# Kernel tuning notes

Hardware: AMD Instinct MI355X
Metric: run time of the kernel (lower is better)

The kernel has to match this reference:

```python
import jax, jax.numpy as jnp
import numpy as np

LOG_EPS = -1000.0
NEG_INF = -1e9  # stand-in for -inf (numerically identical in fp32 LSE, grad-safe)
NOISE_SCALE = 2.0


def setup_inputs() -> dict:
    key = jax.random.key(0)
    ks = jax.random.split(key, 8)
    B, I, J = 2, 64, 512
    Dt, Dm, A = 512, 80, 128
    return {
        "text_embeddings": jax.random.normal(ks[0], (B, I, Dt), jnp.float32),
        "mel_embeddings": jax.random.normal(ks[1], (B, J, Dm), jnp.float32),
        "noise": jax.random.normal(ks[2], (B, I, J), jnp.float32),
        "text_mask": jnp.ones((B, I), dtype=bool),
        "mel_mask": jnp.ones((B, J), dtype=bool),
        "mel_w": jax.random.normal(ks[3], (A, Dm), jnp.float32) * 0.05,
        "mel_b": jax.random.normal(ks[4], (A,), jnp.float32) * 0.05,
        "text_w": jax.random.normal(ks[5], (A, Dt), jnp.float32) * 0.05,
        "v_w": jax.random.normal(ks[6], (A,), jnp.float32) * (1.0 / np.sqrt(A)),
        "v_b": jax.random.normal(ks[7], (1,), jnp.float32) * 0.05,
    }


def _forward(text_embeddings, mel_embeddings, noise, text_mask, mel_mask,
             mel_w, mel_b, text_w, v_w, v_b):
    B, I, _ = text_embeddings.shape
    J = mel_embeddings.shape[1]
    lse = jax.nn.logsumexp

    # --- energy: additive tanh attention + sigmoid(energy + noise) -> (B, I, J)
    pm = mel_embeddings @ mel_w.T + mel_b              # (B, J, A)
    pt = text_embeddings @ text_w.T                    # (B, I, A)
    energy = jnp.tanh(pm[:, None, :, :] + pt[:, :, None, :]) @ v_w + v_b[0]
    energy = jax.nn.sigmoid(energy + noise * NOISE_SCALE)

    # --- log conditional prob P(B_i = j | B_{i-1} = k): (B, I, J, K=J)
    jj = jnp.arange(J)
    tri = jj[:, None] <= jj[None, :]                   # invalid where j <= k (monotone boundaries)
    invalid = (tri[None, None]
               | ~text_mask[:, :, None, None]
               | ~mel_mask[:, None, :, None]
               | ~mel_mask[:, None, None, :])
    e4 = jnp.where(invalid, LOG_EPS, energy[..., None])
    lcp = e4 - lse(e4, axis=2, keepdims=True)          # normalize over j
    # P(B_i >= j | B_{i-1} = k): reversed cumulative logsumexp over j
    geq = jnp.flip(jax.lax.cumlogsumexp(jnp.flip(lcp, 2), axis=2), 2)
    geq = jnp.where(invalid, LOG_EPS, geq)

    # --- forward DP in log domain: B_ij of shape (B, I+1, J+1)
    Jm = (mel_mask.sum(1) - text_mask.sum(1)).max()
    row0 = jnp.full((B, J + 1), NEG_INF).at[:, 0].set(0.0)
    jcol = jnp.arange(J + 1)[None, :]

    def step(prev, xs):
        i, lcp_i = xs                                   # lcp_i: (B, J, K)
        contrib = lse(prev[:, None, :-1] + lcp_i, axis=-1)   # (B, J), fills cols 1..J
        row = jnp.concatenate([jnp.full((B, 1), NEG_INF), contrib], axis=1)
        row = jnp.where((jcol >= i) & (jcol < Jm + i + 2), row, NEG_INF)
        return row, row

    _, rows = jax.lax.scan(step, row0,
                           (jnp.arange(1, I + 1), jnp.swapaxes(lcp, 0, 1)))
    Bij = jnp.concatenate([row0[:, None, :], jnp.swapaxes(rows, 0, 1)], axis=1)

    # --- interval probability P(B_{i-1} < j <= B_i): (B, I, J)
    prob = Bij[:, :-1, :-1]                             # log P(B_{i-1} = k)
    soft = lse(prob[:, :, :, None] + jnp.swapaxes(geq, 2, 3), axis=2)

    # --- expanded text embeddings: (B, J, D_text)
    align_mask = text_mask[:, :, None] & mel_mask[:, None, :]
    expanded = jnp.einsum('bij,bid->bjd', jnp.exp(soft) * align_mask, text_embeddings)
    return soft, expanded


def reference(text_embeddings, mel_embeddings, noise, text_mask, mel_mask,
              mel_w, mel_b, text_w, v_w, v_b):
    return _forward(text_embeddings, mel_embeddings, noise, text_mask, mel_mask,
                    mel_w, mel_b, text_w, v_w, v_b)
```

## Files before the change

kernel.cpp:

```cpp
#include <hip/hip_runtime.h>
#include <math.h>

#define NB 2
#define NI 64
#define NJ 512
#define NDT 512
#define NDM 80
#define NA 128

#define NEG9    (-1000000000.0f)
#define LOGEPS  (-1000.0f)
#define IDENT   (-1.0e30f)
#define LN512   (6.2383246250f)
#define LN2F    (0.69314718056f)
#define INVLN2  (1.44269504089f)
#define LOGEPS2 (-1442.6950409f)

__device__ __forceinline__ float lse2(float a, float b) {
    float m = fmaxf(a, b);
    float d = fabsf(a - b);
    return m + __logf(1.0f + __expf(-d));
}

struct Pair { float m, s; };

__device__ __forceinline__ Pair pcomb(Pair a, Pair b) {
    float mm = fmaxf(a.m, b.m);
    float e  = exp2f(-fabsf(a.m - b.m));
    bool agt = a.m >= b.m;
    float hi = agt ? a.s : b.s;
    float lo = agt ? b.s : a.s;
    return {mm, fmaf(lo, e, hi)};
}

template<int CTRL, int RM>
__device__ __forceinline__ float dpp_lse(float s) {
    int v = __builtin_amdgcn_update_dpp(__float_as_int(IDENT), __float_as_int(s),
                                        CTRL, RM, 0xf, false);
    return lse2(s, __int_as_float(v));
}
template<int CTRL, int RM>
__device__ __forceinline__ Pair dpp_pcomb(Pair x) {
    int bm = __builtin_amdgcn_update_dpp(__float_as_int(IDENT), __float_as_int(x.m),
                                         CTRL, RM, 0xf, false);
    int bs = __builtin_amdgcn_update_dpp(0, __float_as_int(x.s),
                                         CTRL, RM, 0xf, false);
    Pair b{__int_as_float(bm), __int_as_float(bs)};
    return pcomb(x, b);
}

__device__ __forceinline__ float wave_lse_scan(float x) {
    x = dpp_lse<0x111, 0xf>(x);
    x = dpp_lse<0x112, 0xf>(x);
    x = dpp_lse<0x114, 0xf>(x);
    x = dpp_lse<0x118, 0xf>(x);
    x = dpp_lse<0x142, 0xa>(x);
    x = dpp_lse<0x143, 0xc>(x);
    return x;
}
__device__ __forceinline__ Pair wave_pair_scan(Pair x) {
    x = dpp_pcomb<0x111, 0xf>(x);
    x = dpp_pcomb<0x112, 0xf>(x);
    x = dpp_pcomb<0x114, 0xf>(x);
    x = dpp_pcomb<0x118, 0xf>(x);
    x = dpp_pcomb<0x142, 0xa>(x);
    x = dpp_pcomb<0x143, 0xc>(x);
    return x;
}

__device__ __forceinline__ float bcast63(float x) {
    return __int_as_float(__builtin_amdgcn_readlane(__float_as_int(x), 63));
}
__device__ __forceinline__ Pair readp63(Pair x) {
    return { __int_as_float(__builtin_amdgcn_readlane(__float_as_int(x.m), 63)),
             __int_as_float(__builtin_amdgcn_readlane(__float_as_int(x.s), 63)) };
}
__device__ __forceinline__ Pair shflup1(Pair x) {
    return { __shfl_up(x.m, 1, 64), __shfl_up(x.s, 1, 64) };
}

__device__ __forceinline__ void sklansky8(const float* q, float* ls) {
    ls[0]=q[0]; ls[2]=q[2]; ls[4]=q[4]; ls[6]=q[6];
    ls[1]=lse2(q[0],q[1]); ls[3]=lse2(q[2],q[3]);
    ls[5]=lse2(q[4],q[5]); ls[7]=lse2(q[6],q[7]);
    ls[2]=lse2(ls[1],ls[2]); ls[3]=lse2(ls[1],ls[3]);
    ls[6]=lse2(ls[5],ls[6]); ls[7]=lse2(ls[5],ls[7]);
    ls[4]=lse2(ls[3],ls[4]); ls[5]=lse2(ls[3],ls[5]);
    ls[6]=lse2(ls[3],ls[6]); ls[7]=lse2(ls[3],ls[7]);
}
__device__ __forceinline__ void sklansky8p(const Pair* q, Pair* ls) {
    ls[0]=q[0]; ls[2]=q[2]; ls[4]=q[4]; ls[6]=q[6];
    ls[1]=pcomb(q[0],q[1]); ls[3]=pcomb(q[2],q[3]);
    ls[5]=pcomb(q[4],q[5]); ls[7]=pcomb(q[6],q[7]);
    ls[2]=pcomb(ls[1],ls[2]); ls[3]=pcomb(ls[1],ls[3]);
    ls[6]=pcomb(ls[5],ls[6]); ls[7]=pcomb(ls[5],ls[7]);
    ls[4]=pcomb(ls[3],ls[4]); ls[5]=pcomb(ls[3],ls[5]);
    ls[6]=pcomb(ls[3],ls[6]); ls[7]=pcomb(ls[3],ls[7]);
}

__global__ __launch_bounds__(128) void k_proj(const float* __restrict__ text,
                                              const float* __restrict__ mel,
                                              const float* __restrict__ mel_w,
                                              const float* __restrict__ mel_b,
                                              const float* __restrict__ text_w,
                                              float* __restrict__ pmT,
                                              float* __restrict__ pt) {
    __shared__ float row[NDT];
    int blk = blockIdx.x;
    int tid = threadIdx.x;
    if (blk < NB * NJ) {
        int b = blk >> 9, j = blk & (NJ - 1);
        if (tid < NDM) row[tid] = mel[(b * NJ + j) * NDM + tid];
        __syncthreads();
        float acc = mel_b[tid];
        #pragma unroll 8
        for (int k = 0; k < NDM; ++k) acc = fmaf(row[k], mel_w[tid * NDM + k], acc);
        pmT[(b * NA + tid) * NJ + j] = acc;
    } else {
        int blk2 = blk - NB * NJ;
        int b = blk2 >> 6, i = blk2 & (NI - 1);
        for (int k = tid; k < NDT; k += 128) row[k] = text[(b * NI + i) * NDT + k];
        __syncthreads();
        float acc = 0.0f;
        #pragma unroll 8
        for (int k = 0; k < NDT; ++k) acc = fmaf(row[k], text_w[tid * NDT + k], acc);
        pt[(b * NI + i) * NA + tid] = acc;
    }
}

__global__ __launch_bounds__(512) void k_energy(const float* __restrict__ pmT,
                                                const float* __restrict__ pt,
                                                const float* __restrict__ v_w,
                                                const float* __restrict__ v_b,
                                                const float* __restrict__ noise,
                                                float* __restrict__ energy) {
    int bi = blockIdx.x;
    int j = threadIdx.x;
    int b = bi >> 6;
    __shared__ float pts[NA];
    __shared__ float vws[NA];
    if (j < NA) { pts[j] = pt[bi * NA + j]; vws[j] = v_w[j]; }
    __syncthreads();
    float acc = 0.0f;
    const float* pmb = pmT + b * NA * NJ + j;
    #pragma unroll 4
    for (int a = 0; a < NA; ++a) {
        float x = pmb[a * NJ] + pts[a];
        float t = __expf(2.0f * x);
        float th = 1.0f - 2.0f / (t + 1.0f);
        acc = fmaf(th, vws[a], acc);
    }
    float x = acc + v_b[0] + 2.0f * noise[bi * NJ + j];
    energy[bi * NJ + j] = 1.0f / (1.0f + __expf(-x));
}

__global__ __launch_bounds__(64) void k_suffix(const float* __restrict__ energy,
                                               float* __restrict__ T,
                                               float* __restrict__ denom) {
    int bi = blockIdx.x;
    int lane = threadIdx.x;
    const float4* er = (const float4*)(energy + bi * NJ);
    float4 v0 = er[lane * 2], v1 = er[lane * 2 + 1];
    float q[8] = {v0.x, v0.y, v0.z, v0.w, v1.x, v1.y, v1.z, v1.w};
    float ss[8];
    ss[7] = q[7];
    #pragma unroll
    for (int t = 6; t >= 0; --t) ss[t] = lse2(q[t], ss[t + 1]);
    float tot = ss[0];
    #pragma unroll
    for (int off = 1; off < 64; off <<= 1) {
        float o = __shfl_down(tot, off, 64);
        if (lane + off < 64) tot = lse2(tot, o);
    }
    float offS = __shfl_down(tot, 1, 64);
    if (lane == 63) offS = IDENT;
    float Tl[8];
    #pragma unroll
    for (int t = 0; t < 8; ++t) Tl[t] = lse2(ss[t], offS);
    float4* Tr = (float4*)(T + bi * NJ);
    Tr[lane * 2]     = make_float4(Tl[0], Tl[1], Tl[2], Tl[3]);
    Tr[lane * 2 + 1] = make_float4(Tl[4], Tl[5], Tl[6], Tl[7]);
    float nextT0 = __shfl_down(Tl[0], 1, 64);
    float dn[8];
    #pragma unroll
    for (int t = 0; t < 7; ++t) dn[t] = Tl[t + 1];
    dn[7] = (lane == 63) ? (LOGEPS + LN512) : nextT0;
    float4* dr = (float4*)(denom + bi * NJ);
    dr[lane * 2]     = make_float4(dn[0], dn[1], dn[2], dn[3]);
    dr[lane * 2 + 1] = make_float4(dn[4], dn[5], dn[6], dn[7]);
}

__global__ __launch_bounds__(64) void k_scan(const float* __restrict__ denom,
                                             const float* __restrict__ energy,
                                             float* __restrict__ prob) {
    int b = blockIdx.x;
    int lane = threadIdx.x;
    int f = lane * 8;
    Pair prev[8];
    #pragma unroll
    for (int t = 0; t < 8; ++t) prev[t] = {NEG9, 1.0f};
    if (lane == 0) prev[0] = {0.0f, 1.0f};
    float* prow = prob + b * NI * NJ;
    {
        float4* pr = (float4*)prow;
        pr[lane * 2]     = make_float4(prev[0].m, prev[1].m, prev[2].m, prev[3].m);
        pr[lane * 2 + 1] = make_float4(prev[4].m, prev[5].m, prev[6].m, prev[7].m);
    }
    const float* dbase = denom + b * NI * NJ;
    const float* ebase = energy + b * NI * NJ;
    float cdn[8], cen[8], ndn[8], nen[8];
    #pragma unroll
    for (int t = 0; t < 8; ++t) {
        cdn[t] = dbase[f + t] * INVLN2;
        cen[t] = ebase[f + t] * INVLN2;
        ndn[t] = dbase[513 + f + t];
        nen[t] = ebase[513 + f + t];
    }
    for (int i = 1; i < NI; ++i) {
        float fd[8], fe[8];
        #pragma unroll
        for (int t = 0; t < 8; ++t) { fd[t] = ndn[t]; fe[t] = nen[t]; }
        if (i <= NI - 3) {
            int base = (i + 1) * (NJ + 1) + f;
            #pragma unroll
            for (int t = 0; t < 8; ++t) { fd[t] = dbase[base + t]; fe[t] = ebase[base + t]; }
        }
        Pair q[8], ls[8];
        #pragma unroll
        for (int t = 0; t < 8; ++t) q[t] = {prev[t].m - cdn[t], prev[t].s};
        sklansky8p(q, ls);
        Pair lin = wave_pair_scan(ls[7]);
        Pair total = readp63(lin);
        Pair offF = shflup1(lin);
        if (lane == 0) offF = {IDENT, 0.0f};
        Pair sfx = {total.m + LOGEPS2, total.s};
        Pair np[8];
        #pragma unroll
        for (int t = 0; t < 8; ++t) {
            Pair Pex = (t == 0) ? offF : pcomb(offF, ls[t - 1]);
            np[t] = pcomb(Pair{cen[t] + Pex.m, Pex.s}, sfx);
        }
        #pragma unroll
        for (int t = 0; t < 8; ++t) {
            int l = f + t;
            bool ok = (l < 450) && (l + i < 512);
            np[t] = ok ? np[t] : Pair{NEG9, 1.0f};
        }
        #pragma unroll
        for (int t = 0; t < 8; ++t) {
            int j = (f + t + i) & (NJ - 1);
            prow[i * NJ + j] = (np[t].m + log2f(np[t].s)) * LN2F;
        }
        #pragma unroll
        for (int t = 0; t < 8; ++t) {
            int bits = __float_as_int(np[t].s);
            int k = (bits >> 23) - 126;
            prev[t].s = __int_as_float(bits - (k << 23));
            prev[t].m = np[t].m + (float)k;
        }
        #pragma unroll
        for (int t = 0; t < 8; ++t) {
            cdn[t] = ndn[t] * INVLN2; cen[t] = nen[t] * INVLN2;
            ndn[t] = fd[t];           nen[t] = fe[t];
        }
    }
}

__global__ __launch_bounds__(64) void k_soft(const float* __restrict__ prob,
                                             const float* __restrict__ denom,
                                             const float* __restrict__ T,
                                             float* __restrict__ soft_out,
                                             float* __restrict__ w) {
    int bi = blockIdx.x;
    int lane = threadIdx.x;
    const float4* pr = (const float4*)(prob + bi * NJ);
    const float4* dr = (const float4*)(denom + bi * NJ);
    const float4* Tr = (const float4*)(T + bi * NJ);
    float4 p0 = pr[lane * 2], p1 = pr[lane * 2 + 1];
    float4 d0 = dr[lane * 2], d1 = dr[lane * 2 + 1];
    float4 t0 = Tr[lane * 2], t1 = Tr[lane * 2 + 1];
    float p[8] = {p0.x, p0.y, p0.z, p0.w, p1.x, p1.y, p1.z, p1.w};
    float dn[8] = {d0.x, d0.y, d0.z, d0.w, d1.x, d1.y, d1.z, d1.w};
    float Tl[8] = {t0.x, t0.y, t0.z, t0.w, t1.x, t1.y, t1.z, t1.w};
    float r[8], ls[8];
    #pragma unroll
    for (int t = 0; t < 8; ++t) r[t] = p[t] - dn[t];
    sklansky8(r, ls);
    float lin = wave_lse_scan(ls[7]);
    float offF = __shfl_up(lin, 1, 64);
    if (lane == 0) offF = IDENT;
    float pA = lse2(lse2(lse2(p[0], p[1]), lse2(p[2], p[3])),
                    lse2(lse2(p[4], p[5]), lse2(p[6], p[7])));
    float ptot = bcast63(wave_lse_scan(pA));
    float sfx = ptot + LOGEPS;
    #pragma unroll
    for (int t = 0; t < 8; ++t) {
        float Pex = (t == 0) ? offF : lse2(offF, ls[t - 1]);
        float s = lse2(Tl[t] + Pex, sfx);
        int jj = lane * 8 + t;
        soft_out[bi * NJ + jj] = s;
        w[bi * NJ + jj] = __expf(s);
    }
}

__global__ __launch_bounds__(512) void k_expand(const float* __restrict__ w,
                                                const float* __restrict__ text,
                                                float* __restrict__ out2) {
    int bj = blockIdx.x;
    int d = threadIdx.x;
    int b = bj >> 9, j = bj & (NJ - 1);
    float acc = 0.0f;
    #pragma unroll 4
    for (int i = 0; i < NI; ++i)
        acc = fmaf(w[(b * NI + i) * NJ + j], text[(b * NI + i) * NDT + d], acc);
    out2[bj * NDT + d] = acc;
}

extern "C" void kernel_launch(void* const* d_in, const int* in_sizes, int n_in,
                              void* d_out, int out_size, void* d_ws, size_t ws_size,
                              hipStream_t stream) {
    const float* text   = (const float*)d_in[0];
    const float* mel    = (const float*)d_in[1];
    const float* noise  = (const float*)d_in[2];
    const float* mel_w  = (const float*)d_in[5];
    const float* mel_b  = (const float*)d_in[6];
    const float* text_w = (const float*)d_in[7];
    const float* v_w    = (const float*)d_in[8];
    const float* v_b    = (const float*)d_in[9];

    float* ws = (float*)d_ws;
    float* pmT    = ws;
    float* pt     = pmT + NB * NA * NJ;
    float* energy = pt + NB * NI * NA;
    float* T      = energy + NB * NI * NJ;
    float* denom  = T + NB * NI * NJ;
    float* prob   = denom + NB * NI * NJ;
    float* w      = prob + NB * NI * NJ;

    float* soft_out = (float*)d_out;
    float* out2     = soft_out + NB * NI * NJ;

    hipLaunchKernelGGL(k_proj,   dim3(NB * NJ + NB * NI), dim3(128), 0, stream,
                       text, mel, mel_w, mel_b, text_w, pmT, pt);
    hipLaunchKernelGGL(k_energy, dim3(NB * NI), dim3(512), 0, stream,
                       pmT, pt, v_w, v_b, noise, energy);
    hipLaunchKernelGGL(k_suffix, dim3(NB * NI), dim3(64), 0, stream,
                       energy, T, denom);
    hipLaunchKernelGGL(k_scan,   dim3(NB), dim3(64), 0, stream,
                       denom, energy, prob);
    hipLaunchKernelGGL(k_soft,   dim3(NB * NI), dim3(64), 0, stream,
                       prob, denom, T, soft_out, w);
    hipLaunchKernelGGL(k_expand, dim3(NB * NJ), dim3(512), 0, stream,
                       w, text, out2);
}
```

Measured before the change: 201.8 us.

## Fuse suffix LSE into energy kernel and streamline serial DP scan stores

Merges the suffix log-sum-exp kernel into the energy kernel using a wave-level pair scan plus a cross-wave shared-memory combine, which removes one launch and the energy reload. The serial DP scan now keeps rows in unshifted coordinates with a lane shuffle for the column shift. It uses aligned float4 loads and stores the mantissa/exponent pair as two arrays, so the per-step log2 and scattered stores leave the critical serial loop. The log conversion moves to k_soft, at the cost of an extra workspace buffer and more bytes written per row.

```diff
diff --git a/kernel.cpp b/kernel.cpp
--- a/kernel.cpp
+++ b/kernel.cpp
@@ -133,12 +133,17 @@
                                                 const float* __restrict__ v_w,
                                                 const float* __restrict__ v_b,
                                                 const float* __restrict__ noise,
-                                                float* __restrict__ energy) {
+                                                float* __restrict__ energy,
+                                                float* __restrict__ T,
+                                                float* __restrict__ denom) {
     int bi = blockIdx.x;
     int j = threadIdx.x;
     int b = bi >> 6;
+    int lane = j & 63, wv = j >> 6;
     __shared__ float pts[NA];
     __shared__ float vws[NA];
+    __shared__ float wtm[8], wts[8];
+    __shared__ float Ta[NJ];
     if (j < NA) { pts[j] = pt[bi * NA + j]; vws[j] = v_w[j]; }
     __syncthreads();
     float acc = 0.0f;
@@ -151,137 +156,127 @@
         acc = fmaf(th, vws[a], acc);
     }
     float x = acc + v_b[0] + 2.0f * noise[bi * NJ + j];
-    energy[bi * NJ + j] = 1.0f / (1.0f + __expf(-x));
-}
-
-__global__ __launch_bounds__(64) void k_suffix(const float* __restrict__ energy,
-                                               float* __restrict__ T,
-                                               float* __restrict__ denom) {
-    int bi = blockIdx.x;
-    int lane = threadIdx.x;
-    const float4* er = (const float4*)(energy + bi * NJ);
-    float4 v0 = er[lane * 2], v1 = er[lane * 2 + 1];
-    float q[8] = {v0.x, v0.y, v0.z, v0.w, v1.x, v1.y, v1.z, v1.w};
-    float ss[8];
-    ss[7] = q[7];
-    #pragma unroll
-    for (int t = 6; t >= 0; --t) ss[t] = lse2(q[t], ss[t + 1]);
-    float tot = ss[0];
-    #pragma unroll
-    for (int off = 1; off < 64; off <<= 1) {
-        float o = __shfl_down(tot, off, 64);
-        if (lane + off < 64) tot = lse2(tot, o);
-    }
-    float offS = __shfl_down(tot, 1, 64);
-    if (lane == 63) offS = IDENT;
-    float Tl[8];
-    #pragma unroll
-    for (int t = 0; t < 8; ++t) Tl[t] = lse2(ss[t], offS);
-    float4* Tr = (float4*)(T + bi * NJ);
-    Tr[lane * 2]     = make_float4(Tl[0], Tl[1], Tl[2], Tl[3]);
-    Tr[lane * 2 + 1] = make_float4(Tl[4], Tl[5], Tl[6], Tl[7]);
-    float nextT0 = __shfl_down(Tl[0], 1, 64);
-    float dn[8];
-    #pragma unroll
-    for (int t = 0; t < 7; ++t) dn[t] = Tl[t + 1];
-    dn[7] = (lane == 63) ? (LOGEPS + LN512) : nextT0;
-    float4* dr = (float4*)(denom + bi * NJ);
-    dr[lane * 2]     = make_float4(dn[0], dn[1], dn[2], dn[3]);
-    dr[lane * 2 + 1] = make_float4(dn[4], dn[5], dn[6], dn[7]);
+    float e = 1.0f / (1.0f + __expf(-x));
+    energy[bi * NJ + j] = e;
+    float el2 = e * INVLN2;
+    float er = __shfl(el2, 63 - lane, 64);
+    Pair pr = wave_pair_scan({er, 1.0f});
+    if (lane == 63) { wtm[wv] = pr.m; wts[wv] = pr.s; }
+    float sfm = __shfl(pr.m, 63 - lane, 64);
+    float sfs = __shfl(pr.s, 63 - lane, 64);
+    __syncthreads();
+    Pair tail = {IDENT, 0.0f};
+    for (int w2 = wv + 1; w2 < 8; ++w2) tail = pcomb(tail, {wtm[w2], wts[w2]});
+    Pair Tp = pcomb({sfm, sfs}, tail);
+    float Tlog = (Tp.m + log2f(Tp.s)) * LN2F;
+    Ta[j] = Tlog;
+    T[bi * NJ + j] = Tlog;
+    __syncthreads();
+    denom[bi * NJ + j] = (j < NJ - 1) ? Ta[j + 1] : (LOGEPS + LN512);
 }
 
 __global__ __launch_bounds__(64) void k_scan(const float* __restrict__ denom,
                                              const float* __restrict__ energy,
-                                             float* __restrict__ prob) {
+                                             float* __restrict__ pmP,
+                                             float* __restrict__ psP) {
     int b = blockIdx.x;
     int lane = threadIdx.x;
-    int f = lane * 8;
     Pair prev[8];
     #pragma unroll
     for (int t = 0; t < 8; ++t) prev[t] = {NEG9, 1.0f};
     if (lane == 0) prev[0] = {0.0f, 1.0f};
-    float* prow = prob + b * NI * NJ;
+    float* pmrow = pmP + b * NI * NJ;
+    float* psrow = psP + b * NI * NJ;
     {
-        float4* pr = (float4*)prow;
-        pr[lane * 2]     = make_float4(prev[0].m, prev[1].m, prev[2].m, prev[3].m);
-        pr[lane * 2 + 1] = make_float4(prev[4].m, prev[5].m, prev[6].m, prev[7].m);
-    }
-    const float* dbase = denom + b * NI * NJ;
-    const float* ebase = energy + b * NI * NJ;
-    float cdn[8], cen[8], ndn[8], nen[8];
-    #pragma unroll
-    for (int t = 0; t < 8; ++t) {
-        cdn[t] = dbase[f + t] * INVLN2;
-        cen[t] = ebase[f + t] * INVLN2;
-        ndn[t] = dbase[513 + f + t];
-        nen[t] = ebase[513 + f + t];
-    }
+        float4* pm = (float4*)pmrow;
+        float4* ps = (float4*)psrow;
+        pm[lane * 2]     = make_float4(prev[0].m, prev[1].m, prev[2].m, prev[3].m);
+        pm[lane * 2 + 1] = make_float4(prev[4].m, prev[5].m, prev[6].m, prev[7].m);
+        ps[lane * 2]     = make_float4(1.0f, 1.0f, 1.0f, 1.0f);
+        ps[lane * 2 + 1] = make_float4(1.0f, 1.0f, 1.0f, 1.0f);
+    }
+    const float4* dp = (const float4*)(denom + b * NI * NJ);
+    const float4* ep = (const float4*)(energy + b * NI * NJ);
+    float4 cd0 = dp[lane * 2], cd1 = dp[lane * 2 + 1];
+    float4 ce0 = ep[lane * 2], ce1 = ep[lane * 2 + 1];
+    float4 nd0 = dp[(NJ >> 2) + lane * 2], nd1 = dp[(NJ >> 2) + lane * 2 + 1];
+    float4 ne0 = ep[(NJ >> 2) + lane * 2], ne1 = ep[(NJ >> 2) + lane * 2 + 1];
     for (int i = 1; i < NI; ++i) {
-        float fd[8], fe[8];
-        #pragma unroll
-        for (int t = 0; t < 8; ++t) { fd[t] = ndn[t]; fe[t] = nen[t]; }
-        if (i <= NI - 3) {
-            int base = (i + 1) * (NJ + 1) + f;
-            #pragma unroll
-            for (int t = 0; t < 8; ++t) { fd[t] = dbase[base + t]; fe[t] = ebase[base + t]; }
+        float4 fd0 = cd0, fd1 = cd1, fe0 = ce0, fe1 = ce1;
+        if (i < NI - 2) {
+            int base = (i + 1) * (NJ >> 2) + lane * 2;
+            fd0 = dp[base]; fd1 = dp[base + 1];
+            fe0 = ep[base]; fe1 = ep[base + 1];
         }
+        float dn[8] = {cd0.x, cd0.y, cd0.z, cd0.w, cd1.x, cd1.y, cd1.z, cd1.w};
+        float en[8] = {ce0.x, ce0.y, ce0.z, ce0.w, ce1.x, ce1.y, ce1.z, ce1.w};
         Pair q[8], ls[8];
         #pragma unroll
-        for (int t = 0; t < 8; ++t) q[t] = {prev[t].m - cdn[t], prev[t].s};
+        for (int t = 0; t < 8; ++t) q[t] = {prev[t].m - dn[t] * INVLN2, prev[t].s};
         sklansky8p(q, ls);
         Pair lin = wave_pair_scan(ls[7]);
         Pair total = readp63(lin);
         Pair offF = shflup1(lin);
         if (lane == 0) offF = {IDENT, 0.0f};
         Pair sfx = {total.m + LOGEPS2, total.s};
-        Pair np[8];
+        Pair contrib[8];
         #pragma unroll
         for (int t = 0; t < 8; ++t) {
             Pair Pex = (t == 0) ? offF : pcomb(offF, ls[t - 1]);
-            np[t] = pcomb(Pair{cen[t] + Pex.m, Pex.s}, sfx);
+            contrib[t] = pcomb(Pair{en[t] * INVLN2 + Pex.m, Pex.s}, sfx);
         }
+        Pair c7 = shflup1(contrib[7]);
+        Pair np[8];
+        np[0] = c7;
+        #pragma unroll
+        for (int t = 1; t < 8; ++t) np[t] = contrib[t - 1];
         #pragma unroll
         for (int t = 0; t < 8; ++t) {
-            int l = f + t;
-            bool ok = (l < 450) && (l + i < 512);
-            np[t] = ok ? np[t] : Pair{NEG9, 1.0f};
+            int j = lane * 8 + t;
+            bool ok = (j >= i) && (j < i + 450);
+            prev[t] = ok ? np[t] : Pair{NEG9, 1.0f};
         }
+        float4* pm = (float4*)(pmrow + i * NJ);
+        float4* ps = (float4*)(psrow + i * NJ);
+        pm[lane * 2]     = make_float4(prev[0].m, prev[1].m, prev[2].m, prev[3].m);
+        pm[lane * 2 + 1] = make_float4(prev[4].m, prev[5].m, prev[6].m, prev[7].m);
+        ps[lane * 2]     = make_float4(prev[0].s, prev[1].s, prev[2].s, prev[3].s);
+        ps[lane * 2 + 1] = make_float4(prev[4].s, prev[5].s, prev[6].s, prev[7].s);
         #pragma unroll
         for (int t = 0; t < 8; ++t) {
-            int j = (f + t + i) & (NJ - 1);
-            prow[i * NJ + j] = (np[t].m + log2f(np[t].s)) * LN2F;
-        }
-        #pragma unroll
-        for (int t = 0; t < 8; ++t) {
-            int bits = __float_as_int(np[t].s);
+            int bits = __float_as_int(prev[t].s);
             int k = (bits >> 23) - 126;
             prev[t].s = __int_as_float(bits - (k << 23));
-            prev[t].m = np[t].m + (float)k;
+            prev[t].m = prev[t].m + (float)k;
         }
-        #pragma unroll
-        for (int t = 0; t < 8; ++t) {
-            cdn[t] = ndn[t] * INVLN2; cen[t] = nen[t] * INVLN2;
-            ndn[t] = fd[t];           nen[t] = fe[t];
-        }
-    }
-}
-
-__global__ __launch_bounds__(64) void k_soft(const float* __restrict__ prob,
+        cd0 = nd0; cd1 = nd1; ce0 = ne0; ce1 = ne1;
+        nd0 = fd0; nd1 = fd1; ne0 = fe0; ne1 = fe1;
+    }
+}
+
+__global__ __launch_bounds__(64) void k_soft(const float* __restrict__ pmP,
+                                             const float* __restrict__ psP,
                                              const float* __restrict__ denom,
                                              const float* __restrict__ T,
                                              float* __restrict__ soft_out,
                                              float* __restrict__ w) {
     int bi = blockIdx.x;
     int lane = threadIdx.x;
-    const float4* pr = (const float4*)(prob + bi * NJ);
+    const float4* pmr = (const float4*)(pmP + bi * NJ);
+    const float4* psr = (const float4*)(psP + bi * NJ);
     const float4* dr = (const float4*)(denom + bi * NJ);
     const float4* Tr = (const float4*)(T + bi * NJ);
-    float4 p0 = pr[lane * 2], p1 = pr[lane * 2 + 1];
+    float4 m0 = pmr[lane * 2], m1 = pmr[lane * 2 + 1];
+    float4 s0 = psr[lane * 2], s1 = psr[lane * 2 + 1];
     float4 d0 = dr[lane * 2], d1 = dr[lane * 2 + 1];
     float4 t0 = Tr[lane * 2], t1 = Tr[lane * 2 + 1];
-    float p[8] = {p0.x, p0.y, p0.z, p0.w, p1.x, p1.y, p1.z, p1.w};
+    float pm[8] = {m0.x, m0.y, m0.z, m0.w, m1.x, m1.y, m1.z, m1.w};
+    float psv[8] = {s0.x, s0.y, s0.z, s0.w, s1.x, s1.y, s1.z, s1.w};
     float dn[8] = {d0.x, d0.y, d0.z, d0.w, d1.x, d1.y, d1.z, d1.w};
     float Tl[8] = {t0.x, t0.y, t0.z, t0.w, t1.x, t1.y, t1.z, t1.w};
+    float p[8];
+    #pragma unroll
+    for (int t = 0; t < 8; ++t) p[t] = (pm[t] + log2f(psv[t])) * LN2F;
     float r[8], ls[8];
     #pragma unroll
     for (int t = 0; t < 8; ++t) r[t] = p[t] - dn[t];
@@ -334,8 +329,9 @@
     float* energy = pt + NB * NI * NA;
     float* T      = energy + NB * NI * NJ;
     float* denom  = T + NB * NI * NJ;
-    float* prob   = denom + NB * NI * NJ;
-    float* w      = prob + NB * NI * NJ;
+    float* pmP    = denom + NB * NI * NJ;
+    float* psP    = pmP + NB * NI * NJ;
+    float* w      = psP + NB * NI * NJ;
 
     float* soft_out = (float*)d_out;
     float* out2     = soft_out + NB * NI * NJ;
@@ -343,13 +339,11 @@
     hipLaunchKernelGGL(k_proj,   dim3(NB * NJ + NB * NI), dim3(128), 0, stream,
                        text, mel, mel_w, mel_b, text_w, pmT, pt);
     hipLaunchKernelGGL(k_energy, dim3(NB * NI), dim3(512), 0, stream,
-                       pmT, pt, v_w, v_b, noise, energy);
-    hipLaunchKernelGGL(k_suffix, dim3(NB * NI), dim3(64), 0, stream,
-                       energy, T, denom);
+                       pmT, pt, v_w, v_b, noise, energy, T, denom);
     hipLaunchKernelGGL(k_scan,   dim3(NB), dim3(64), 0, stream,
-                       denom, energy, prob);
+                       denom, energy, pmP, psP);
     hipLaunchKernelGGL(k_soft,   dim3(NB * NI), dim3(64), 0, stream,
-                       prob, denom, T, soft_out, w);
+                       pmP, psP, denom, T, soft_out, w);
     hipLaunchKernelGGL(k_expand, dim3(NB * NJ), dim3(512), 0, stream,
                        w, text, out2);
 }
```

Measured after the change: 189.6 us. 1.06x faster.
